# Performance work log

Hardware: AMD Instinct MI355X
Metric: run time of the kernel (lower is better)

Reference implementation:

```python
import jax, jax.numpy as jnp
import numpy as np
from jax import lax

UNITS_OSC = 512
STEPS = 100
DT = 0.001
ACTION_DIM = 256
BATCH = 256


def complex_dense(zc, Wr, Wi, br, bi):
    # zc: [B, 2n] = concat(real, imag); complex matmul with relu on both parts
    n = Wr.shape[0]
    xr, xi = zc[:, :n], zc[:, n:]
    yr = jax.nn.relu(xr @ Wr - xi @ Wi + br)
    yi = jax.nn.relu(xr @ Wi + xi @ Wr + bi)
    return jnp.concatenate([yr, yi], axis=-1)


def hopf_step(zc, omega, mu, b):
    # zc: [B, 2*UNITS_OSC]; Hopf dynamics dz = ((mu - |z|^2) + i*k*omega) z + b, Euler step
    x, y = zc[:, :UNITS_OSC], zc[:, UNITS_OSC:]
    r2 = x * x + y * y
    w = omega * jnp.arange(1, UNITS_OSC + 1, dtype=zc.dtype)  # [B, UNITS_OSC]
    nx = x + DT * ((mu - r2) * x - w * y + b)
    ny = y + DT * ((mu - r2) * y + w * x)
    return jnp.concatenate([nx, ny], axis=-1)


def _dense_init(key, fan_in, fan_out):
    return jax.random.normal(key, (fan_in, fan_out), dtype=jnp.float32) / np.sqrt(fan_in)


def setup_inputs() -> dict:
    key = jax.random.key(0)
    ks = jax.random.split(key, 16)
    inp = {
        'motion_state': jax.random.normal(ks[0], (BATCH, 64), dtype=jnp.float32),
        'robot_state': jax.random.normal(ks[1], (BATCH, 128), dtype=jnp.float32),
        'z': 0.1 * jax.random.normal(ks[2], (BATCH, 2 * UNITS_OSC), dtype=jnp.float32),
        'W_ms': _dense_init(ks[3], 64, 256), 'b_ms': jnp.zeros((256,), jnp.float32),
        'W_rs': _dense_init(ks[4], 128, 256), 'b_rs': jnp.zeros((256,), jnp.float32),
        'W_cmb': _dense_init(ks[5], 512, 512), 'b_cmb': jnp.zeros((512,), jnp.float32),
        'W_om': _dense_init(ks[6], 512, 1), 'b_om': jnp.zeros((1,), jnp.float32),
        'W_mu': _dense_init(ks[7], 512, 512), 'b_mu': jnp.zeros((512,), jnp.float32),
        'W_b': _dense_init(ks[8], 512, 512), 'b_b': jnp.zeros((512,), jnp.float32),
        'Wr0': _dense_init(ks[9], 512, 1024), 'Wi0': _dense_init(ks[10], 512, 1024),
        'br0': jnp.zeros((1024,), jnp.float32), 'bi0': jnp.zeros((1024,), jnp.float32),
        'Wr1': _dense_init(ks[11], 1024, 512), 'Wi1': _dense_init(ks[12], 1024, 512),
        'br1': jnp.zeros((512,), jnp.float32), 'bi1': jnp.zeros((512,), jnp.float32),
        'Wr2': _dense_init(ks[13], 512, 256), 'Wi2': _dense_init(ks[14], 512, 256),
        'br2': jnp.zeros((256,), jnp.float32), 'bi2': jnp.zeros((256,), jnp.float32),
    }
    return inp


def reference(motion_state, robot_state, z,
              W_ms, b_ms, W_rs, b_rs, W_cmb, b_cmb, W_om, b_om, W_mu, b_mu, W_b, b_b,
              Wr0, Wi0, br0, bi0, Wr1, Wi1, br1, bi1, Wr2, Wi2, br2, bi2):
    # --- StateEncoder ---
    ms = jax.nn.relu(motion_state @ W_ms + b_ms)
    rs = jax.nn.relu(robot_state @ W_rs + b_rs)
    st = jax.nn.relu(jnp.concatenate([ms, rs], axis=-1) @ W_cmb + b_cmb)
    omega = jnp.abs(jax.nn.relu(st @ W_om + b_om))   # [B, 1]
    mu = jnp.abs(jax.nn.relu(st @ W_mu + b_mu))      # [B, UNITS_OSC]
    bb = jnp.abs(jax.nn.relu(st @ W_b + b_b))        # [B, UNITS_OSC]

    def mlp(zc):
        zc = complex_dense(zc, Wr0, Wi0, br0, bi0)
        zc = complex_dense(zc, Wr1, Wi1, br1, bi1)
        return complex_dense(zc, Wr2, Wi2, br2, bi2)  # [B, 2*ACTION_DIM]

    # first oscillator step (this z is the z_out returned by the original module)
    z_out = hopf_step(z, omega, mu, bb)
    o0 = mlp(z_out)

    def body(zc, _):
        zn = hopf_step(zc, omega, mu, bb)
        return zn, mlp(zn)

    _, os = lax.scan(body, z_out, None, length=STEPS - 1)   # [STEPS-1, B, 2A]
    out = jnp.concatenate([o0[None], os], axis=0)           # [STEPS, B, 2A]
    out = jnp.transpose(out, (1, 0, 2))[:, :, :ACTION_DIM]  # [B, STEPS, A]
    return out, z_out, omega, mu, bb
```

## Files before the change

### kernel.cpp

```cpp
#include <hip/hip_runtime.h>
#include <hip/hip_bf16.h>

#define STEPS 100
#define DTC 0.001f

typedef __attribute__((ext_vector_type(8))) short bf16x8;
typedef __attribute__((ext_vector_type(4))) float f32x4;

__device__ __forceinline__ void gload16(const void* g, void* l) {
  __builtin_amdgcn_global_load_lds(
      (const __attribute__((address_space(1))) void*)g,
      (__attribute__((address_space(3))) void*)l,
      16, 0, 0);
}


__global__ __launch_bounds__(512)
void front(const float* __restrict__ ms_in, const float* __restrict__ rs_in,
           const float* __restrict__ z,
           const float* __restrict__ Wms, const float* __restrict__ bms,
           const float* __restrict__ Wrs, const float* __restrict__ brs,
           const float* __restrict__ Wc, const float* __restrict__ bc,
           const float* __restrict__ Wmu, const float* __restrict__ bmu,
           const float* __restrict__ Wb, const float* __restrict__ bbias,
           const float* __restrict__ Wom, const float* __restrict__ bom,
           __hip_bfloat16* __restrict__ A0, float* __restrict__ z_out,
           float* __restrict__ om_out, float* __restrict__ mu_out,
           float* __restrict__ bb_out) {
  const int b = blockIdx.x;
  const int n = threadIdx.x;
  __shared__ float sIn[192];
  __shared__ float stA[512];
  __shared__ float stB[512];
  if (n < 64) sIn[n] = ms_in[b * 64 + n];
  else if (n < 192) sIn[n] = rs_in[b * 128 + (n - 64)];
  __syncthreads();
  float a1;
  if (n < 256) {
    a1 = bms[n];
    for (int k = 0; k < 64; ++k) a1 += sIn[k] * Wms[k * 256 + n];
  } else {
    int nn = n - 256;
    a1 = brs[nn];
    for (int k = 0; k < 128; ++k) a1 += sIn[64 + k] * Wrs[k * 256 + nn];
  }
  stA[n] = fmaxf(a1, 0.f);
  __syncthreads();
  float a2 = bc[n];
  for (int k = 0; k < 512; ++k) a2 += stA[k] * Wc[k * 512 + n];
  stB[n] = fmaxf(a2, 0.f);
  __syncthreads();
  float am = bmu[n], ab = bbias[n];
  for (int k = 0; k < 512; ++k) {
    float sv = stB[k];
    am += sv * Wmu[k * 512 + n];
    ab += sv * Wb[k * 512 + n];
  }
  const float muv = fabsf(fmaxf(am, 0.f));
  const float bbv = fabsf(fmaxf(ab, 0.f));
  mu_out[b * 512 + n] = muv;
  bb_out[b * 512 + n] = bbv;
  stA[n] = stB[n] * Wom[n];
  __syncthreads();
  for (int off = 256; off > 0; off >>= 1) {
    if (n < off) stA[n] += stA[n + off];
    __syncthreads();
  }
  const float om = fabsf(fmaxf(stA[0] + bom[0], 0.f));
  if (n == 0) om_out[b] = om;
  float x = z[b * 1024 + n];
  float y = z[b * 1024 + 512 + n];
  const float w = om * (float)(n + 1);
  for (int t = 0; t < STEPS; ++t) {
    float r2 = x * x + y * y;
    float g = muv - r2;
    float nx = x + DTC * (g * x - w * y + bbv);
    float ny = y + DTC * (g * y + w * x);
    x = nx; y = ny;
    if (t == 0) {
      z_out[b * 1024 + n] = x;
      z_out[b * 1024 + 512 + n] = y;
    }
    size_t row = (size_t)b * STEPS + t;
    A0[row * 1024 + n] = __float2bfloat16(x);
    A0[row * 1024 + 512 + n] = __float2bfloat16(y);
  }
}


__constant__ int    jSrcC[10] = {0, 1, 1, 0, 2, 3, 3, 2, 4, 5};
__constant__ float  jSgnC[10] = {1.f, 1.f, -1.f, 1.f, 1.f, 1.f, -1.f, 1.f, 1.f, -1.f};
__constant__ int    jCC[10]   = {1024, 1024, 1024, 1024, 512, 512, 512, 512, 256, 256};
__constant__ int    jDstC[10] = {0, 0, 0, 0, 1, 1, 1, 1, 2, 2};
__constant__ int    jDsC[10]  = {1024, 1024, 1024, 1024, 2048, 2048, 2048, 2048, 1024, 1024};
__constant__ long   jOffC[10] = {0, 1048576, 512, 1049088, 0, 1048576, 1024, 1049600, 0, 512};

__global__ void tpack_all(const float* __restrict__ Wr0, const float* __restrict__ Wi0,
                          const float* __restrict__ Wr1, const float* __restrict__ Wi1,
                          const float* __restrict__ Wr2, const float* __restrict__ Wi2,
                          __hip_bfloat16* __restrict__ BT0, __hip_bfloat16* __restrict__ BT1,
                          __hip_bfloat16* __restrict__ BT2) {
  __shared__ float tile[32][33];
  const int bid = blockIdx.x;
  int j, w;
  if (bid < 4096) { j = bid >> 9; w = bid & 511; }
  else            { j = 8 + ((bid - 4096) >> 7); w = (bid - 4096) & 127; }
  const float* srcs[6] = {Wr0, Wi0, Wr1, Wi1, Wr2, Wi2};
  __hip_bfloat16* dsts[3] = {BT0, BT1, BT2};
  const float* src = srcs[jSrcC[j]];
  __hip_bfloat16* dst = dsts[jDstC[j]] + jOffC[j];
  const int C = jCC[j], ds = jDsC[j];
  const float sign = jSgnC[j];
  const int ncb = C >> 5;
  const int cb = (w % ncb) * 32, rb = (w / ncb) * 32;
  const int tx = threadIdx.x, ty = threadIdx.y;
#pragma unroll
  for (int i = 0; i < 32; i += 8)
    tile[ty + i][tx] = src[(size_t)(rb + ty + i) * C + (cb + tx)];
  __syncthreads();
#pragma unroll
  for (int i = 0; i < 32; i += 8)
    dst[(size_t)(cb + ty + i) * ds + (rb + tx)] = __float2bfloat16(sign * tile[tx][ty + i]);
}


#define SBAR __builtin_amdgcn_sched_barrier(0)

#define RD_A(DST, QX, cb) do { _Pragma("unroll") for (int mi = 0; mi < 5; ++mi) \
  DST[mi] = *(const bf16x8*)((cb) + (abase ^ ((QX) * 64)) + mi * 2048); } while (0)

#define RD_B(DST, h, QX, cb) do { _Pragma("unroll") for (int jj = 0; jj < 2; ++jj) \
  DST[jj] = *(const bf16x8*)((cb) + (bbase ^ ((QX) * 64)) + (2 * (h) + jj) * 2048); } while (0)

#define MF_PH(ASET, BSET, h) do { _Pragma("unroll") for (int mi = 0; mi < 5; ++mi) \
  _Pragma("unroll") for (int jj = 0; jj < 2; ++jj) \
    acc[mi][2 * (h) + jj] = __builtin_amdgcn_mfma_f32_16x16x32_bf16( \
        ASET[mi], BSET[jj], acc[mi][2 * (h) + jj], 0, 0, 0); } while (0)

template <int OUT_BF16>
__global__ __launch_bounds__(256, 2)
void gemm160(const __hip_bfloat16* __restrict__ A, const __hip_bfloat16* __restrict__ BT,
             const float* __restrict__ biasA, const float* __restrict__ biasB, int bsplit,
             void* __restrict__ Cout, int N, int K, int ntn_l2) {
  extern __shared__ char lds[];

  const int tid = threadIdx.x;
  const int lane = tid & 63;
  const int wid = tid >> 6;
  const int wr = wid >> 1;
  const int wc = wid & 1;
  const int fr = lane & 15, fq = lane >> 4;

  const int nwg = gridDim.x;
  int f = blockIdx.x;
  f = (f & 7) * (nwg >> 3) + (f >> 3);
  const int m0 = (f >> ntn_l2) * 160;
  const int n0 = (f & ((1 << ntn_l2) - 1)) << 7;

  const int rA = tid >> 3;
  const int c8v = (tid & 7) ^ (rA & 7);
  const __hip_bfloat16* Asrc = A + (size_t)(m0 + rA) * K + c8v * 8;
  const __hip_bfloat16* Bsrc = BT + (size_t)(n0 + rA) * K + c8v * 8;

  const int x0 = fq ^ (fr & 7);
  const int abase = (wr * 80 + fr) * 128 + x0 * 16;
  const int bbase = 20480 + (wc * 64 + fr) * 128 + x0 * 16;

  auto stgA = [&](int j, int ko, char* buf) {
    gload16(Asrc + ko + (size_t)32 * j * K, buf + j * 4096 + wid * 1024);
  };
  auto stgB = [&](int j, int ko, char* buf) {
    gload16(Bsrc + ko + (size_t)32 * j * K, buf + 20480 + j * 4096 + wid * 1024);
  };

  stgA(0, 0, lds); stgA(1, 0, lds); stgA(2, 0, lds); stgA(3, 0, lds); stgA(4, 0, lds);
  stgB(0, 0, lds); stgB(1, 0, lds); stgB(2, 0, lds); stgB(3, 0, lds);

  f32x4 acc[5][4] = {};
  bf16x8 a0[5], a1[5], b00[2], b10[2], b01[2], b11[2];

  const int nk = K >> 6;
  for (int kt = 0; kt < nk - 1; ++kt) {
    char* cb = lds + (kt & 1) * 36864;
    char* nb = lds + ((kt & 1) ^ 1) * 36864;
    const int ko = (kt + 1) << 6;
    __builtin_amdgcn_s_barrier();
    SBAR;
    stgA(0, ko, nb); stgA(1, ko, nb);
    SBAR;
    asm volatile("s_waitcnt vmcnt(2)" ::: "memory");
    __builtin_amdgcn_s_barrier();
    SBAR;
    RD_A(a0, 0, cb);
    RD_B(b00, 0, 0, cb);
    SBAR;
    RD_B(b10, 1, 0, cb);
    asm volatile("s_waitcnt lgkmcnt(2)" ::: "memory");
    SBAR;
    __builtin_amdgcn_s_setprio(1); MF_PH(a0, b00, 0); __builtin_amdgcn_s_setprio(0);
    __builtin_amdgcn_s_barrier();
    SBAR;
    stgA(2, ko, nb); stgA(3, ko, nb); stgA(4, ko, nb);
    RD_A(a1, 1, cb);
    RD_B(b01, 0, 1, cb);
    asm volatile("s_waitcnt lgkmcnt(7)" ::: "memory");
    SBAR;
    __builtin_amdgcn_s_setprio(1); MF_PH(a0, b10, 1); __builtin_amdgcn_s_setprio(0);
    __builtin_amdgcn_s_barrier();
    SBAR;
    stgB(0, ko, nb); stgB(1, ko, nb);
    RD_B(b11, 1, 1, cb);
    asm volatile("s_waitcnt lgkmcnt(2)" ::: "memory");
    SBAR;
    __builtin_amdgcn_s_setprio(1); MF_PH(a1, b01, 0); __builtin_amdgcn_s_setprio(0);
    __builtin_amdgcn_s_barrier();
    SBAR;
    stgB(2, ko, nb); stgB(3, ko, nb);
    asm volatile("s_waitcnt lgkmcnt(0)" ::: "memory");
    SBAR;
    __builtin_amdgcn_s_setprio(1); MF_PH(a1, b11, 1); __builtin_amdgcn_s_setprio(0);
  }
  {
    char* cb = lds + ((nk - 1) & 1) * 36864;
    __builtin_amdgcn_s_barrier();
    asm volatile("s_waitcnt vmcnt(0)" ::: "memory");
    __builtin_amdgcn_s_barrier();
    SBAR;
    RD_A(a0, 0, cb);
    RD_B(b00, 0, 0, cb);
    SBAR;
    RD_B(b10, 1, 0, cb);
    asm volatile("s_waitcnt lgkmcnt(2)" ::: "memory");
    SBAR;
    __builtin_amdgcn_s_setprio(1); MF_PH(a0, b00, 0); __builtin_amdgcn_s_setprio(0);
    RD_A(a1, 1, cb);
    RD_B(b01, 0, 1, cb);
    asm volatile("s_waitcnt lgkmcnt(7)" ::: "memory");
    SBAR;
    __builtin_amdgcn_s_setprio(1); MF_PH(a0, b10, 1); __builtin_amdgcn_s_setprio(0);
    RD_B(b11, 1, 1, cb);
    asm volatile("s_waitcnt lgkmcnt(2)" ::: "memory");
    SBAR;
    __builtin_amdgcn_s_setprio(1); MF_PH(a1, b01, 0); __builtin_amdgcn_s_setprio(0);
    asm volatile("s_waitcnt lgkmcnt(0)" ::: "memory");
    SBAR;
    __builtin_amdgcn_s_setprio(1); MF_PH(a1, b11, 1); __builtin_amdgcn_s_setprio(0);
  }

#pragma unroll
  for (int nj = 0; nj < 4; ++nj) {
    const int col = n0 + wc * 64 + nj * 16 + fr;
    const float bv = (col < bsplit) ? biasA[col] : biasB[col - bsplit];
#pragma unroll
    for (int mi = 0; mi < 5; ++mi) {
#pragma unroll
      for (int r = 0; r < 4; ++r) {
        const int row = m0 + wr * 80 + mi * 16 + fq * 4 + r;
        float v = fmaxf(acc[mi][nj][r] + bv, 0.f);
        if (OUT_BF16)
          ((__hip_bfloat16*)Cout)[(size_t)row * N + col] = __float2bfloat16(v);
        else
          ((float*)Cout)[(size_t)row * N + col] = v;
      }
    }
  }
}


extern "C" void kernel_launch(void* const* d_in, const int* in_sizes, int n_in,
                              void* d_out, int out_size, void* d_ws, size_t ws_size,
                              hipStream_t stream) {
  const float* motion = (const float*)d_in[0];
  const float* robot  = (const float*)d_in[1];
  const float* z      = (const float*)d_in[2];
  const float* W_ms   = (const float*)d_in[3];
  const float* b_ms   = (const float*)d_in[4];
  const float* W_rs   = (const float*)d_in[5];
  const float* b_rs   = (const float*)d_in[6];
  const float* W_cmb  = (const float*)d_in[7];
  const float* b_cmb  = (const float*)d_in[8];
  const float* W_om   = (const float*)d_in[9];
  const float* b_om   = (const float*)d_in[10];
  const float* W_mu   = (const float*)d_in[11];
  const float* b_mu   = (const float*)d_in[12];
  const float* W_b    = (const float*)d_in[13];
  const float* b_b    = (const float*)d_in[14];
  const float* Wr0    = (const float*)d_in[15];
  const float* Wi0    = (const float*)d_in[16];
  const float* br0    = (const float*)d_in[17];
  const float* bi0    = (const float*)d_in[18];
  const float* Wr1    = (const float*)d_in[19];
  const float* Wi1    = (const float*)d_in[20];
  const float* br1    = (const float*)d_in[21];
  const float* bi1    = (const float*)d_in[22];
  const float* Wr2    = (const float*)d_in[23];
  const float* Wi2    = (const float*)d_in[24];
  const float* br2    = (const float*)d_in[25];

  float* out  = (float*)d_out;
  float* zout = out + (size_t)6553600;
  float* omg  = zout + 262144;
  float* muo  = omg + 256;
  float* bbo  = muo + 131072;

  char* ws = (char*)d_ws;
  __hip_bfloat16* BT0 = (__hip_bfloat16*)ws;
  __hip_bfloat16* BT1 = BT0 + (size_t)2048 * 1024;
  __hip_bfloat16* BT2 = BT1 + (size_t)1024 * 2048;
  __hip_bfloat16* A0  = BT2 + (size_t)256 * 1024;
  __hip_bfloat16* C1  = A0 + (size_t)25600 * 1024;
  __hip_bfloat16* C2  = C1 + (size_t)25600 * 2048;

  front<<<256, 512, 0, stream>>>(motion, robot, z, W_ms, b_ms, W_rs, b_rs,
                                 W_cmb, b_cmb, W_mu, b_mu, W_b, b_b, W_om, b_om,
                                 A0, zout, omg, muo, bbo);

  tpack_all<<<4352, dim3(32, 8), 0, stream>>>(Wr0, Wi0, Wr1, Wi1, Wr2, Wi2,
                                              BT0, BT1, BT2);

  gemm160<1><<<2560, 256, 73728, stream>>>(A0, BT0, br0, bi0, 1024, C1, 2048, 1024, 4);
  gemm160<1><<<1280, 256, 73728, stream>>>(C1, BT1, br1, bi1, 512, C2, 1024, 2048, 3);
  gemm160<0><<<320, 256, 73728, stream>>>(C2, BT2, br2, br2, 256, out, 256, 1024, 1);
}
```

Baseline: 298.5 us.

## Merge encoder and weight-pack kernels into one launch, batch four rows per block

Combines the state-encoder/oscillator kernel and the weight transpose-pack kernel into a single launch, so the first 64 blocks run the encoder and the rest do packing concurrently. Each encoder block now handles four batch rows, so every weight load is reused four times and encoder weight traffic drops. Transpose blocks now use 512 threads in place of 256, each block still covering one 32x32 tile. The cost is fewer, heavier encoder blocks (64 instead of 256), which could lengthen that critical path, and a larger shared-memory footprint for the whole kernel.

```diff
diff --git a/kernel.cpp b/kernel.cpp
--- a/kernel.cpp
+++ b/kernel.cpp
@@ -15,79 +15,6 @@
 }
 
 
-__global__ __launch_bounds__(512)
-void front(const float* __restrict__ ms_in, const float* __restrict__ rs_in,
-           const float* __restrict__ z,
-           const float* __restrict__ Wms, const float* __restrict__ bms,
-           const float* __restrict__ Wrs, const float* __restrict__ brs,
-           const float* __restrict__ Wc, const float* __restrict__ bc,
-           const float* __restrict__ Wmu, const float* __restrict__ bmu,
-           const float* __restrict__ Wb, const float* __restrict__ bbias,
-           const float* __restrict__ Wom, const float* __restrict__ bom,
-           __hip_bfloat16* __restrict__ A0, float* __restrict__ z_out,
-           float* __restrict__ om_out, float* __restrict__ mu_out,
-           float* __restrict__ bb_out) {
-  const int b = blockIdx.x;
-  const int n = threadIdx.x;
-  __shared__ float sIn[192];
-  __shared__ float stA[512];
-  __shared__ float stB[512];
-  if (n < 64) sIn[n] = ms_in[b * 64 + n];
-  else if (n < 192) sIn[n] = rs_in[b * 128 + (n - 64)];
-  __syncthreads();
-  float a1;
-  if (n < 256) {
-    a1 = bms[n];
-    for (int k = 0; k < 64; ++k) a1 += sIn[k] * Wms[k * 256 + n];
-  } else {
-    int nn = n - 256;
-    a1 = brs[nn];
-    for (int k = 0; k < 128; ++k) a1 += sIn[64 + k] * Wrs[k * 256 + nn];
-  }
-  stA[n] = fmaxf(a1, 0.f);
-  __syncthreads();
-  float a2 = bc[n];
-  for (int k = 0; k < 512; ++k) a2 += stA[k] * Wc[k * 512 + n];
-  stB[n] = fmaxf(a2, 0.f);
-  __syncthreads();
-  float am = bmu[n], ab = bbias[n];
-  for (int k = 0; k < 512; ++k) {
-    float sv = stB[k];
-    am += sv * Wmu[k * 512 + n];
-    ab += sv * Wb[k * 512 + n];
-  }
-  const float muv = fabsf(fmaxf(am, 0.f));
-  const float bbv = fabsf(fmaxf(ab, 0.f));
-  mu_out[b * 512 + n] = muv;
-  bb_out[b * 512 + n] = bbv;
-  stA[n] = stB[n] * Wom[n];
-  __syncthreads();
-  for (int off = 256; off > 0; off >>= 1) {
-    if (n < off) stA[n] += stA[n + off];
-    __syncthreads();
-  }
-  const float om = fabsf(fmaxf(stA[0] + bom[0], 0.f));
-  if (n == 0) om_out[b] = om;
-  float x = z[b * 1024 + n];
-  float y = z[b * 1024 + 512 + n];
-  const float w = om * (float)(n + 1);
-  for (int t = 0; t < STEPS; ++t) {
-    float r2 = x * x + y * y;
-    float g = muv - r2;
-    float nx = x + DTC * (g * x - w * y + bbv);
-    float ny = y + DTC * (g * y + w * x);
-    x = nx; y = ny;
-    if (t == 0) {
-      z_out[b * 1024 + n] = x;
-      z_out[b * 1024 + 512 + n] = y;
-    }
-    size_t row = (size_t)b * STEPS + t;
-    A0[row * 1024 + n] = __float2bfloat16(x);
-    A0[row * 1024 + 512 + n] = __float2bfloat16(y);
-  }
-}
-
-
 __constant__ int    jSrcC[10] = {0, 1, 1, 0, 2, 3, 3, 2, 4, 5};
 __constant__ float  jSgnC[10] = {1.f, 1.f, -1.f, 1.f, 1.f, 1.f, -1.f, 1.f, 1.f, -1.f};
 __constant__ int    jCC[10]   = {1024, 1024, 1024, 1024, 512, 512, 512, 512, 256, 256};
@@ -95,32 +22,165 @@
 __constant__ int    jDsC[10]  = {1024, 1024, 1024, 1024, 2048, 2048, 2048, 2048, 1024, 1024};
 __constant__ long   jOffC[10] = {0, 1048576, 512, 1049088, 0, 1048576, 1024, 1049600, 0, 512};
 
-__global__ void tpack_all(const float* __restrict__ Wr0, const float* __restrict__ Wi0,
-                          const float* __restrict__ Wr1, const float* __restrict__ Wi1,
-                          const float* __restrict__ Wr2, const float* __restrict__ Wi2,
-                          __hip_bfloat16* __restrict__ BT0, __hip_bfloat16* __restrict__ BT1,
-                          __hip_bfloat16* __restrict__ BT2) {
-  __shared__ float tile[32][33];
+__global__ __launch_bounds__(512)
+void prep(const float* __restrict__ ms_in, const float* __restrict__ rs_in,
+          const float* __restrict__ z,
+          const float* __restrict__ Wms, const float* __restrict__ bms,
+          const float* __restrict__ Wrs, const float* __restrict__ brs,
+          const float* __restrict__ Wc, const float* __restrict__ bc,
+          const float* __restrict__ Wmu, const float* __restrict__ bmu,
+          const float* __restrict__ Wb, const float* __restrict__ bbias,
+          const float* __restrict__ Wom, const float* __restrict__ bom,
+          const float* __restrict__ Wr0, const float* __restrict__ Wi0,
+          const float* __restrict__ Wr1, const float* __restrict__ Wi1,
+          const float* __restrict__ Wr2, const float* __restrict__ Wi2,
+          __hip_bfloat16* __restrict__ BT0, __hip_bfloat16* __restrict__ BT1,
+          __hip_bfloat16* __restrict__ BT2,
+          __hip_bfloat16* __restrict__ A0, float* __restrict__ z_out,
+          float* __restrict__ om_out, float* __restrict__ mu_out,
+          float* __restrict__ bb_out) {
   const int bid = blockIdx.x;
-  int j, w;
-  if (bid < 4096) { j = bid >> 9; w = bid & 511; }
-  else            { j = 8 + ((bid - 4096) >> 7); w = (bid - 4096) & 127; }
-  const float* srcs[6] = {Wr0, Wi0, Wr1, Wi1, Wr2, Wi2};
-  __hip_bfloat16* dsts[3] = {BT0, BT1, BT2};
-  const float* src = srcs[jSrcC[j]];
-  __hip_bfloat16* dst = dsts[jDstC[j]] + jOffC[j];
-  const int C = jCC[j], ds = jDsC[j];
-  const float sign = jSgnC[j];
-  const int ncb = C >> 5;
-  const int cb = (w % ncb) * 32, rb = (w / ncb) * 32;
-  const int tx = threadIdx.x, ty = threadIdx.y;
-#pragma unroll
-  for (int i = 0; i < 32; i += 8)
-    tile[ty + i][tx] = src[(size_t)(rb + ty + i) * C + (cb + tx)];
-  __syncthreads();
-#pragma unroll
-  for (int i = 0; i < 32; i += 8)
-    dst[(size_t)(cb + ty + i) * ds + (rb + tx)] = __float2bfloat16(sign * tile[tx][ty + i]);
+  const int tid = threadIdx.x;
+
+  if (bid < 64) {
+    __shared__ float sIn[4][192];
+    __shared__ float stA[4][512];
+    __shared__ float stB[4][512];
+    const int b4 = bid * 4;
+    const int n = tid;
+#pragma unroll
+    for (int r = 0; r < 4; ++r) {
+      if (n < 64) sIn[r][n] = ms_in[(b4 + r) * 64 + n];
+      else if (n < 192) sIn[r][n] = rs_in[(b4 + r) * 128 + (n - 64)];
+    }
+    __syncthreads();
+    float a[4];
+    if (n < 256) {
+      const float bias = bms[n];
+#pragma unroll
+      for (int r = 0; r < 4; ++r) a[r] = bias;
+      for (int k = 0; k < 64; ++k) {
+        const float wv = Wms[k * 256 + n];
+#pragma unroll
+        for (int r = 0; r < 4; ++r) a[r] += sIn[r][k] * wv;
+      }
+    } else {
+      const int nn = n - 256;
+      const float bias = brs[nn];
+#pragma unroll
+      for (int r = 0; r < 4; ++r) a[r] = bias;
+      for (int k = 0; k < 128; ++k) {
+        const float wv = Wrs[k * 256 + nn];
+#pragma unroll
+        for (int r = 0; r < 4; ++r) a[r] += sIn[r][64 + k] * wv;
+      }
+    }
+#pragma unroll
+    for (int r = 0; r < 4; ++r) stA[r][n] = fmaxf(a[r], 0.f);
+    __syncthreads();
+    float c[4];
+    {
+      const float bias = bc[n];
+#pragma unroll
+      for (int r = 0; r < 4; ++r) c[r] = bias;
+      for (int k = 0; k < 512; ++k) {
+        const float wv = Wc[k * 512 + n];
+#pragma unroll
+        for (int r = 0; r < 4; ++r) c[r] += stA[r][k] * wv;
+      }
+    }
+#pragma unroll
+    for (int r = 0; r < 4; ++r) stB[r][n] = fmaxf(c[r], 0.f);
+    __syncthreads();
+    float am[4], ab[4];
+    {
+      const float bm = bmu[n], bb2 = bbias[n];
+#pragma unroll
+      for (int r = 0; r < 4; ++r) { am[r] = bm; ab[r] = bb2; }
+      for (int k = 0; k < 512; ++k) {
+        const float wm = Wmu[k * 512 + n];
+        const float wb = Wb[k * 512 + n];
+#pragma unroll
+        for (int r = 0; r < 4; ++r) {
+          am[r] += stB[r][k] * wm;
+          ab[r] += stB[r][k] * wb;
+        }
+      }
+    }
+    float muv[4], bbv[4];
+#pragma unroll
+    for (int r = 0; r < 4; ++r) {
+      muv[r] = fabsf(fmaxf(am[r], 0.f));
+      bbv[r] = fabsf(fmaxf(ab[r], 0.f));
+      mu_out[(b4 + r) * 512 + n] = muv[r];
+      bb_out[(b4 + r) * 512 + n] = bbv[r];
+    }
+    {
+      const float wo = Wom[n];
+#pragma unroll
+      for (int r = 0; r < 4; ++r) stA[r][n] = stB[r][n] * wo;
+    }
+    __syncthreads();
+    for (int off = 256; off > 0; off >>= 1) {
+      if (n < off) {
+#pragma unroll
+        for (int r = 0; r < 4; ++r) stA[r][n] += stA[r][n + off];
+      }
+      __syncthreads();
+    }
+    float om[4];
+#pragma unroll
+    for (int r = 0; r < 4; ++r) {
+      om[r] = fabsf(fmaxf(stA[r][0] + bom[0], 0.f));
+      if (n == 0) om_out[b4 + r] = om[r];
+    }
+    float xx[4], yy[4], ww[4];
+#pragma unroll
+    for (int r = 0; r < 4; ++r) {
+      xx[r] = z[(b4 + r) * 1024 + n];
+      yy[r] = z[(b4 + r) * 1024 + 512 + n];
+      ww[r] = om[r] * (float)(n + 1);
+    }
+    for (int t = 0; t < STEPS; ++t) {
+#pragma unroll
+      for (int r = 0; r < 4; ++r) {
+        const float r2 = xx[r] * xx[r] + yy[r] * yy[r];
+        const float g = muv[r] - r2;
+        const float nx = xx[r] + DTC * (g * xx[r] - ww[r] * yy[r] + bbv[r]);
+        const float ny = yy[r] + DTC * (g * yy[r] + ww[r] * xx[r]);
+        xx[r] = nx; yy[r] = ny;
+        if (t == 0) {
+          z_out[(b4 + r) * 1024 + n] = nx;
+          z_out[(b4 + r) * 1024 + 512 + n] = ny;
+        }
+        const size_t row = (size_t)(b4 + r) * STEPS + t;
+        A0[row * 1024 + n] = __float2bfloat16(nx);
+        A0[row * 1024 + 512 + n] = __float2bfloat16(ny);
+      }
+    }
+  } else {
+    __shared__ float tile[32][33];
+    const int t = bid - 64;
+    int j, w;
+    if (t < 4096) { j = t >> 9; w = t & 511; }
+    else          { j = 8 + ((t - 4096) >> 7); w = (t - 4096) & 127; }
+    const float* srcs[6] = {Wr0, Wi0, Wr1, Wi1, Wr2, Wi2};
+    __hip_bfloat16* dsts[3] = {BT0, BT1, BT2};
+    const float* src = srcs[jSrcC[j]];
+    __hip_bfloat16* dst = dsts[jDstC[j]] + jOffC[j];
+    const int C = jCC[j], ds = jDsC[j];
+    const float sign = jSgnC[j];
+    const int ncb = C >> 5;
+    const int cb = (w % ncb) * 32, rb = (w / ncb) * 32;
+    const int tx = tid & 31, ty = tid >> 5;
+#pragma unroll
+    for (int i = 0; i < 32; i += 16)
+      tile[ty + i][tx] = src[(size_t)(rb + ty + i) * C + (cb + tx)];
+    __syncthreads();
+#pragma unroll
+    for (int i = 0; i < 32; i += 16)
+      dst[(size_t)(cb + ty + i) * ds + (rb + tx)] = __float2bfloat16(sign * tile[tx][ty + i]);
+  }
 }
 
 
@@ -311,12 +371,10 @@
   __hip_bfloat16* C1  = A0 + (size_t)25600 * 1024;
   __hip_bfloat16* C2  = C1 + (size_t)25600 * 2048;
 
-  front<<<256, 512, 0, stream>>>(motion, robot, z, W_ms, b_ms, W_rs, b_rs,
+  prep<<<4416, 512, 0, stream>>>(motion, robot, z, W_ms, b_ms, W_rs, b_rs,
                                  W_cmb, b_cmb, W_mu, b_mu, W_b, b_b, W_om, b_om,
+                                 Wr0, Wi0, Wr1, Wi1, Wr2, Wi2, BT0, BT1, BT2,
                                  A0, zout, omg, muo, bbo);
-
-  tpack_all<<<4352, dim3(32, 8), 0, stream>>>(Wr0, Wi0, Wr1, Wi1, Wr2, Wi2,
-                                              BT0, BT1, BT2);
 
   gemm160<1><<<2560, 256, 73728, stream>>>(A0, BT0, br0, bi0, 1024, C1, 2048, 1024, 4);
   gemm160<1><<<1280, 256, 73728, stream>>>(C1, BT1, br1, bi1, 512, C2, 1024, 2048, 3);
```

Result: slower. 394.6 us (+32.2%).

## Merge front encoder and weight transpose into one prep kernel with split-K

Applied to the files above, without the earlier changes.

Combines the state-encoder/oscillator kernel and the weight transpose-pack kernel into a single launch, with blocks dispatched by index. Encoder blocks now use 1024 threads and split each 512-long reduction across two halves, combining partial sums through shared memory. This is meant to cut launch overhead, let the transpose work overlap the latency-bound encoder, and shorten the serial dot-product loops. The cost is extra barriers and shared memory, and transpose blocks move from 256 to 1024 threads, which may change occupancy.

```diff
diff --git a/kernel.cpp b/kernel.cpp
--- a/kernel.cpp
+++ b/kernel.cpp
@@ -15,79 +15,6 @@
 }
 
 
-__global__ __launch_bounds__(512)
-void front(const float* __restrict__ ms_in, const float* __restrict__ rs_in,
-           const float* __restrict__ z,
-           const float* __restrict__ Wms, const float* __restrict__ bms,
-           const float* __restrict__ Wrs, const float* __restrict__ brs,
-           const float* __restrict__ Wc, const float* __restrict__ bc,
-           const float* __restrict__ Wmu, const float* __restrict__ bmu,
-           const float* __restrict__ Wb, const float* __restrict__ bbias,
-           const float* __restrict__ Wom, const float* __restrict__ bom,
-           __hip_bfloat16* __restrict__ A0, float* __restrict__ z_out,
-           float* __restrict__ om_out, float* __restrict__ mu_out,
-           float* __restrict__ bb_out) {
-  const int b = blockIdx.x;
-  const int n = threadIdx.x;
-  __shared__ float sIn[192];
-  __shared__ float stA[512];
-  __shared__ float stB[512];
-  if (n < 64) sIn[n] = ms_in[b * 64 + n];
-  else if (n < 192) sIn[n] = rs_in[b * 128 + (n - 64)];
-  __syncthreads();
-  float a1;
-  if (n < 256) {
-    a1 = bms[n];
-    for (int k = 0; k < 64; ++k) a1 += sIn[k] * Wms[k * 256 + n];
-  } else {
-    int nn = n - 256;
-    a1 = brs[nn];
-    for (int k = 0; k < 128; ++k) a1 += sIn[64 + k] * Wrs[k * 256 + nn];
-  }
-  stA[n] = fmaxf(a1, 0.f);
-  __syncthreads();
-  float a2 = bc[n];
-  for (int k = 0; k < 512; ++k) a2 += stA[k] * Wc[k * 512 + n];
-  stB[n] = fmaxf(a2, 0.f);
-  __syncthreads();
-  float am = bmu[n], ab = bbias[n];
-  for (int k = 0; k < 512; ++k) {
-    float sv = stB[k];
-    am += sv * Wmu[k * 512 + n];
-    ab += sv * Wb[k * 512 + n];
-  }
-  const float muv = fabsf(fmaxf(am, 0.f));
-  const float bbv = fabsf(fmaxf(ab, 0.f));
-  mu_out[b * 512 + n] = muv;
-  bb_out[b * 512 + n] = bbv;
-  stA[n] = stB[n] * Wom[n];
-  __syncthreads();
-  for (int off = 256; off > 0; off >>= 1) {
-    if (n < off) stA[n] += stA[n + off];
-    __syncthreads();
-  }
-  const float om = fabsf(fmaxf(stA[0] + bom[0], 0.f));
-  if (n == 0) om_out[b] = om;
-  float x = z[b * 1024 + n];
-  float y = z[b * 1024 + 512 + n];
-  const float w = om * (float)(n + 1);
-  for (int t = 0; t < STEPS; ++t) {
-    float r2 = x * x + y * y;
-    float g = muv - r2;
-    float nx = x + DTC * (g * x - w * y + bbv);
-    float ny = y + DTC * (g * y + w * x);
-    x = nx; y = ny;
-    if (t == 0) {
-      z_out[b * 1024 + n] = x;
-      z_out[b * 1024 + 512 + n] = y;
-    }
-    size_t row = (size_t)b * STEPS + t;
-    A0[row * 1024 + n] = __float2bfloat16(x);
-    A0[row * 1024 + 512 + n] = __float2bfloat16(y);
-  }
-}
-
-
 __constant__ int    jSrcC[10] = {0, 1, 1, 0, 2, 3, 3, 2, 4, 5};
 __constant__ float  jSgnC[10] = {1.f, 1.f, -1.f, 1.f, 1.f, 1.f, -1.f, 1.f, 1.f, -1.f};
 __constant__ int    jCC[10]   = {1024, 1024, 1024, 1024, 512, 512, 512, 512, 256, 256};
@@ -95,32 +22,129 @@
 __constant__ int    jDsC[10]  = {1024, 1024, 1024, 1024, 2048, 2048, 2048, 2048, 1024, 1024};
 __constant__ long   jOffC[10] = {0, 1048576, 512, 1049088, 0, 1048576, 1024, 1049600, 0, 512};
 
-__global__ void tpack_all(const float* __restrict__ Wr0, const float* __restrict__ Wi0,
-                          const float* __restrict__ Wr1, const float* __restrict__ Wi1,
-                          const float* __restrict__ Wr2, const float* __restrict__ Wi2,
-                          __hip_bfloat16* __restrict__ BT0, __hip_bfloat16* __restrict__ BT1,
-                          __hip_bfloat16* __restrict__ BT2) {
-  __shared__ float tile[32][33];
+__global__ __launch_bounds__(1024)
+void prep(const float* __restrict__ ms_in, const float* __restrict__ rs_in,
+          const float* __restrict__ z,
+          const float* __restrict__ Wms, const float* __restrict__ bms,
+          const float* __restrict__ Wrs, const float* __restrict__ brs,
+          const float* __restrict__ Wc, const float* __restrict__ bc,
+          const float* __restrict__ Wmu, const float* __restrict__ bmu,
+          const float* __restrict__ Wb, const float* __restrict__ bbias,
+          const float* __restrict__ Wom, const float* __restrict__ bom,
+          const float* __restrict__ Wr0, const float* __restrict__ Wi0,
+          const float* __restrict__ Wr1, const float* __restrict__ Wi1,
+          const float* __restrict__ Wr2, const float* __restrict__ Wi2,
+          __hip_bfloat16* __restrict__ BT0, __hip_bfloat16* __restrict__ BT1,
+          __hip_bfloat16* __restrict__ BT2,
+          __hip_bfloat16* __restrict__ A0, float* __restrict__ z_out,
+          float* __restrict__ om_out, float* __restrict__ mu_out,
+          float* __restrict__ bb_out) {
   const int bid = blockIdx.x;
-  int j, w;
-  if (bid < 4096) { j = bid >> 9; w = bid & 511; }
-  else            { j = 8 + ((bid - 4096) >> 7); w = (bid - 4096) & 127; }
-  const float* srcs[6] = {Wr0, Wi0, Wr1, Wi1, Wr2, Wi2};
-  __hip_bfloat16* dsts[3] = {BT0, BT1, BT2};
-  const float* src = srcs[jSrcC[j]];
-  __hip_bfloat16* dst = dsts[jDstC[j]] + jOffC[j];
-  const int C = jCC[j], ds = jDsC[j];
-  const float sign = jSgnC[j];
-  const int ncb = C >> 5;
-  const int cb = (w % ncb) * 32, rb = (w / ncb) * 32;
-  const int tx = threadIdx.x, ty = threadIdx.y;
-#pragma unroll
-  for (int i = 0; i < 32; i += 8)
-    tile[ty + i][tx] = src[(size_t)(rb + ty + i) * C + (cb + tx)];
-  __syncthreads();
-#pragma unroll
-  for (int i = 0; i < 32; i += 8)
-    dst[(size_t)(cb + ty + i) * ds + (rb + tx)] = __float2bfloat16(sign * tile[tx][ty + i]);
+  const int tid = threadIdx.x;
+
+  if (bid < 256) {
+    __shared__ float sIn[192];
+    __shared__ float stA[512];
+    __shared__ float stB[512];
+    __shared__ float pA[2][512];
+    __shared__ float pB[2][512];
+    const int b = bid;
+    const int n = tid & 511;
+    const int h = tid >> 9;
+    if (h == 0) {
+      if (n < 64) sIn[n] = ms_in[b * 64 + n];
+      else if (n < 192) sIn[n] = rs_in[b * 128 + (n - 64)];
+    }
+    __syncthreads();
+    if (h == 0) {
+      float a1;
+      if (n < 256) {
+        a1 = bms[n];
+        for (int k = 0; k < 64; ++k) a1 += sIn[k] * Wms[k * 256 + n];
+      } else {
+        const int nn = n - 256;
+        a1 = brs[nn];
+        for (int k = 0; k < 128; ++k) a1 += sIn[64 + k] * Wrs[k * 256 + nn];
+      }
+      stA[n] = fmaxf(a1, 0.f);
+    }
+    __syncthreads();
+    {
+      float p = (h == 0) ? bc[n] : 0.f;
+      const int k0 = h << 8;
+      for (int k = 0; k < 256; ++k) p += stA[k0 + k] * Wc[(k0 + k) * 512 + n];
+      pA[h][n] = p;
+    }
+    __syncthreads();
+    if (h == 0) stB[n] = fmaxf(pA[0][n] + pA[1][n], 0.f);
+    __syncthreads();
+    {
+      float pm = (h == 0) ? bmu[n] : 0.f;
+      float pb = (h == 0) ? bbias[n] : 0.f;
+      const int k0 = h << 8;
+      for (int k = 0; k < 256; ++k) {
+        const float sv = stB[k0 + k];
+        pm += sv * Wmu[(k0 + k) * 512 + n];
+        pb += sv * Wb[(k0 + k) * 512 + n];
+      }
+      pA[h][n] = pm;
+      pB[h][n] = pb;
+    }
+    __syncthreads();
+    float muv = 0.f, bbv = 0.f;
+    if (h == 0) {
+      muv = fabsf(fmaxf(pA[0][n] + pA[1][n], 0.f));
+      bbv = fabsf(fmaxf(pB[0][n] + pB[1][n], 0.f));
+      mu_out[b * 512 + n] = muv;
+      bb_out[b * 512 + n] = bbv;
+    }
+    __syncthreads();
+    if (h == 0) pA[0][n] = stB[n] * Wom[n];
+    __syncthreads();
+    for (int off = 256; off > 0; off >>= 1) {
+      if (h == 0 && n < off) pA[0][n] += pA[0][n + off];
+      __syncthreads();
+    }
+    const float om = fabsf(fmaxf(pA[0][0] + bom[0], 0.f));
+    if (tid == 0) om_out[b] = om;
+    if (h == 0) {
+      float x = z[b * 1024 + n];
+      float y = z[b * 1024 + 512 + n];
+      const float w = om * (float)(n + 1);
+      for (int t = 0; t < STEPS; ++t) {
+        const float r2 = x * x + y * y;
+        const float g = muv - r2;
+        const float nx = x + DTC * (g * x - w * y + bbv);
+        const float ny = y + DTC * (g * y + w * x);
+        x = nx; y = ny;
+        if (t == 0) {
+          z_out[b * 1024 + n] = x;
+          z_out[b * 1024 + 512 + n] = y;
+        }
+        const size_t row = (size_t)b * STEPS + t;
+        A0[row * 1024 + n] = __float2bfloat16(x);
+        A0[row * 1024 + 512 + n] = __float2bfloat16(y);
+      }
+    }
+  } else {
+    __shared__ float tile[32][33];
+    const int t = bid - 256;
+    int j, w;
+    if (t < 4096) { j = t >> 9; w = t & 511; }
+    else          { j = 8 + ((t - 4096) >> 7); w = (t - 4096) & 127; }
+    const float* srcs[6] = {Wr0, Wi0, Wr1, Wi1, Wr2, Wi2};
+    __hip_bfloat16* dsts[3] = {BT0, BT1, BT2};
+    const float* src = srcs[jSrcC[j]];
+    __hip_bfloat16* dst = dsts[jDstC[j]] + jOffC[j];
+    const int C = jCC[j], ds = jDsC[j];
+    const float sign = jSgnC[j];
+    const int ncb = C >> 5;
+    const int cb = (w % ncb) * 32, rb = (w / ncb) * 32;
+    const int tx = tid & 31, ty = tid >> 5;
+    tile[ty][tx] = src[(size_t)(rb + ty) * C + (cb + tx)];
+    __syncthreads();
+    dst[(size_t)(cb + ty) * ds + (rb + tx)] = __float2bfloat16(sign * tile[tx][ty]);
+  }
 }
 
 
@@ -311,12 +335,10 @@
   __hip_bfloat16* C1  = A0 + (size_t)25600 * 1024;
   __hip_bfloat16* C2  = C1 + (size_t)25600 * 2048;
 
-  front<<<256, 512, 0, stream>>>(motion, robot, z, W_ms, b_ms, W_rs, b_rs,
-                                 W_cmb, b_cmb, W_mu, b_mu, W_b, b_b, W_om, b_om,
-                                 A0, zout, omg, muo, bbo);
-
-  tpack_all<<<4352, dim3(32, 8), 0, stream>>>(Wr0, Wi0, Wr1, Wi1, Wr2, Wi2,
-                                              BT0, BT1, BT2);
+  prep<<<4608, 1024, 0, stream>>>(motion, robot, z, W_ms, b_ms, W_rs, b_rs,
+                                  W_cmb, b_cmb, W_mu, b_mu, W_b, b_b, W_om, b_om,
+                                  Wr0, Wi0, Wr1, Wi1, Wr2, Wi2, BT0, BT1, BT2,
+                                  A0, zout, omg, muo, bbo);
 
   gemm160<1><<<2560, 256, 73728, stream>>>(A0, BT0, br0, bi0, 1024, C1, 2048, 1024, 4);
   gemm160<1><<<1280, 256, 73728, stream>>>(C1, BT1, br1, bi1, 512, C2, 1024, 2048, 3);
```

New measurement: 271.9 us. 8.9% less time.
